# Performance work log

Hardware: AMD Instinct MI355X
Metric: run time of the kernel (lower is better)

## Reference

```python
import jax, jax.numpy as jnp
import numpy as np

NHEAD = 16
HEAD_DIM = 64
ROPE_BASE = 10000.0


def _rotate_half(x):
    # interleaved convention: pairs (x0,x1)->(-x1,x0)
    x1 = x[..., ::2]
    x2 = x[..., 1::2]
    return jnp.stack([-x2, x1], axis=-1).reshape(x.shape)


def _rope_cache(seq_len, head_dim, base):
    half = head_dim // 2
    inv_freq = 1.0 / base ** (jnp.arange(half, dtype=jnp.float32) / float(half))
    t = jnp.arange(seq_len, dtype=jnp.float32)
    freqs = jnp.einsum('i,j->ij', t, inv_freq)          # [T, half]
    emb = jnp.concatenate([freqs, freqs], axis=-1)      # [T, D] (half-half cat, matches torch source)
    return jnp.cos(emb), jnp.sin(emb)


def setup_inputs() -> dict:
    key = jax.random.key(0)
    k1, k2, k3 = jax.random.split(key, 3)
    b, t, c = 2, 2048, 1024
    x = jax.random.normal(k1, (b, t, c), dtype=jnp.float32)
    # torch nn.Linear weights: [out_features, in_features], scaled like kaiming-uniform-ish
    W_qkv = jax.random.normal(k2, (3 * c, c), dtype=jnp.float32) / np.sqrt(c)
    W_out = jax.random.normal(k3, (c, c), dtype=jnp.float32) / np.sqrt(c)
    return {"x": x, "W_qkv": W_qkv, "W_out": W_out}


def reference(x, W_qkv, W_out):
    b, t, c = x.shape
    nh, hd = NHEAD, HEAD_DIM
    qkv = x @ W_qkv.T                                   # [b, t, 3c]
    q, k, v = jnp.split(qkv, 3, axis=-1)

    def to_heads(a):
        return a.reshape(b, t, nh, hd).transpose(0, 2, 1, 3)  # [b, nh, t, hd]

    q, k, v = to_heads(q), to_heads(k), to_heads(v)
    cos, sin = _rope_cache(t, hd, ROPE_BASE)            # [t, hd]
    cos = cos.astype(q.dtype)[None, None]
    sin = sin.astype(q.dtype)[None, None]
    q = q * cos + _rotate_half(q) * sin
    k = k * cos + _rotate_half(k) * sin

    scale = 1.0 / np.sqrt(hd).astype(np.float32)
    scores = jnp.einsum('bhqd,bhkd->bhqk', q, k) * scale
    attn = jax.nn.softmax(scores, axis=-1)
    y = jnp.einsum('bhqk,bhkd->bhqd', attn, v)          # [b, nh, t, hd]
    y = y.transpose(0, 2, 1, 3).reshape(b, t, c)
    return y @ W_out.T
```

## Files before the change

### kernel.cpp

```cpp
#include <hip/hip_runtime.h>
#include <hip/hip_bf16.h>
#include <math.h>

typedef __hip_bfloat16 bf16;
typedef _Float16 f16;
typedef __attribute__((ext_vector_type(8))) short bf16x8;
typedef __attribute__((ext_vector_type(8))) _Float16 f16x8;
typedef __attribute__((ext_vector_type(4))) float f32x4;
typedef __attribute__((ext_vector_type(4))) unsigned u32x4;

#define MFMA_BF(a,b,c) __builtin_amdgcn_mfma_f32_16x16x32_bf16((a),(b),(c),0,0,0)
#define MFMA_F16(a,b,c) __builtin_amdgcn_mfma_f32_16x16x32_f16((a),(b),(c),0,0,0)

__device__ __forceinline__ void load_lds16(const void* g, void* l) {
  __builtin_amdgcn_global_load_lds(
      (__attribute__((address_space(1))) void*)(g),
      (__attribute__((address_space(3))) void*)(l), 16, 0, 0);
}

__device__ __forceinline__ unsigned pk_bf16(float a, float b) {
  unsigned ua = __builtin_bit_cast(unsigned, a);
  unsigned ub = __builtin_bit_cast(unsigned, b);
  ua += 0x7fffu + ((ua >> 16) & 1u);
  ub += 0x7fffu + ((ub >> 16) & 1u);
  return (ua >> 16) | (ub & 0xffff0000u);
}

__global__ void cvt_all(const float* __restrict__ x, const float* __restrict__ wq,
                        const float* __restrict__ wo, unsigned* __restrict__ xb,
                        unsigned* __restrict__ wqb, unsigned* __restrict__ wob) {
  int i = blockIdx.x * blockDim.x + threadIdx.x;
  const float* src;
  unsigned* dst;
  int off;
  if (i < 1048576) { src = x; dst = xb; off = i; }
  else if (i < 1048576 + 786432) { src = wq; dst = wqb; off = i - 1048576; }
  else { src = wo; dst = wob; off = i - (1048576 + 786432); }
  float4 v = reinterpret_cast<const float4*>(src)[off];
  uint2 u;
  u.x = pk_bf16(v.x, v.y);
  u.y = pk_bf16(v.z, v.w);
  reinterpret_cast<uint2*>(dst)[off] = u;
}

__global__ __launch_bounds__(256, 2)
void gemm_qkv(const bf16* __restrict__ A, const bf16* __restrict__ B,
              bf16* __restrict__ outq, bf16* __restrict__ outk,
              f16* __restrict__ outv) {
  __shared__ __align__(16) bf16 As[128 * 32];
  __shared__ __align__(16) bf16 Bs[128 * 32];
  const int K = 1024;
  const int tid = threadIdx.x;
  const int w = tid >> 6;
  const int lane = tid & 63;
  const int quad = lane >> 4;
  const int col = lane & 15;
  const int waveM = w >> 1;
  const int waveN = w & 1;
  const int bm = blockIdx.y * 128;
  const int bn = blockIdx.x * 128;

  f32x4 acc[4][4] = {};
  const int srow = lane >> 2;
  const int skoff = (lane & 3) * 8;

  for (int k0 = 0; k0 < K; k0 += 32) {
    __syncthreads();
#pragma unroll
    for (int p = 0; p < 2; ++p) {
      int r = p * 64 + w * 16 + srow;
      load_lds16(A + (size_t)(bm + r) * K + k0 + skoff, (char*)As + p * 4096 + w * 1024);
      load_lds16(B + (size_t)(bn + r) * K + k0 + skoff, (char*)Bs + p * 4096 + w * 1024);
    }
    __syncthreads();
    bf16x8 af[4], bfr[4];
#pragma unroll
    for (int i = 0; i < 4; ++i)
      af[i] = *reinterpret_cast<const bf16x8*>(As + (waveM * 64 + i * 16 + col) * 32 + quad * 8);
#pragma unroll
    for (int j = 0; j < 4; ++j)
      bfr[j] = *reinterpret_cast<const bf16x8*>(Bs + (waveN * 64 + j * 16 + col) * 32 + quad * 8);
#pragma unroll
    for (int i = 0; i < 4; ++i)
#pragma unroll
      for (int j = 0; j < 4; ++j)
        acc[i][j] = MFMA_BF(af[i], bfr[j], acc[i][j]);
  }

  if (bn < 2048) {
    const float NEGK = -0.4152410118f;
    const float C1 = 0.1803368799f;
    const float sgn = (col & 1) ? 1.0f : -1.0f;
#pragma unroll
    for (int j = 0; j < 4; ++j) {
      const int n0 = bn + waveN * 64 + j * 16;
      const int sel = n0 >> 10;
      const int hh = (n0 & 1023) >> 6;
      const int dd = (n0 & 63) + col;
      bf16* outp = sel ? outk : outq;
      const float post = sel ? 1.0f : C1;
      const float invf = __builtin_amdgcn_exp2f((float)((n0 & 31) + col) * NEGK);
#pragma unroll
      for (int i = 0; i < 4; ++i) {
#pragma unroll
        for (int r = 0; r < 4; ++r) {
          int m = bm + waveM * 64 + i * 16 + quad * 4 + r;
          int b = m >> 11, t = m & 2047;
          float v = acc[i][j][r];
          float partner = __shfl_xor(v, 1);
          float ang = (float)t * invf;
          float res = (v * __cosf(ang) + sgn * partner * __sinf(ang)) * post;
          outp[((size_t)(b * 16 + hh) * 2048 + t) * 64 + dd] = __float2bfloat16(res);
        }
      }
    }
  } else {
    const int b = bm >> 11;
    const int tt0 = (bm & 2047) + waveM * 64;
#pragma unroll
    for (int j = 0; j < 4; ++j) {
      const int n0 = bn + waveN * 64 + j * 16;
      const int hh = (n0 & 1023) >> 6;
      const int dd = (n0 & 63) + col;
      f16* dst = outv + (size_t)(b * 16 + hh) * 131072 + (size_t)dd * 2048;
#pragma unroll
      for (int i = 0; i < 4; ++i) {
        uint2 pk;
        pk.x = __builtin_bit_cast(unsigned, __builtin_amdgcn_cvt_pkrtz(acc[i][j][0], acc[i][j][1]));
        pk.y = __builtin_bit_cast(unsigned, __builtin_amdgcn_cvt_pkrtz(acc[i][j][2], acc[i][j][3]));
        *reinterpret_cast<uint2*>(dst + tt0 + i * 16 + quad * 4) = pk;
      }
    }
  }
}

__global__ __launch_bounds__(256, 2)
void gemm_out(const bf16* __restrict__ A, const bf16* __restrict__ B,
              float* __restrict__ outf) {
  __shared__ __align__(16) bf16 As[64 * 32];
  __shared__ __align__(16) bf16 Bs[128 * 32];
  const int K = 1024;
  const int tid = threadIdx.x;
  const int w = tid >> 6;
  const int lane = tid & 63;
  const int quad = lane >> 4;
  const int col = lane & 15;
  const int bm = blockIdx.y * 64;
  const int bn = blockIdx.x * 128;

  f32x4 acc[4][2] = {};
  const int srow = lane >> 2;
  const int skoff = (lane & 3) * 8;

  for (int k0 = 0; k0 < K; k0 += 32) {
    __syncthreads();
    load_lds16(A + (size_t)(bm + w * 16 + srow) * K + k0 + skoff, (char*)As + w * 1024);
#pragma unroll
    for (int p = 0; p < 2; ++p)
      load_lds16(B + (size_t)(bn + p * 64 + w * 16 + srow) * K + k0 + skoff,
                 (char*)Bs + p * 4096 + w * 1024);
    __syncthreads();
    bf16x8 af[4], bfr[2];
#pragma unroll
    for (int i = 0; i < 4; ++i)
      af[i] = *reinterpret_cast<const bf16x8*>(As + (i * 16 + col) * 32 + quad * 8);
#pragma unroll
    for (int j = 0; j < 2; ++j)
      bfr[j] = *reinterpret_cast<const bf16x8*>(Bs + (w * 32 + j * 16 + col) * 32 + quad * 8);
#pragma unroll
    for (int i = 0; i < 4; ++i)
#pragma unroll
      for (int j = 0; j < 2; ++j)
        acc[i][j] = MFMA_BF(af[i], bfr[j], acc[i][j]);
  }

#pragma unroll
  for (int i = 0; i < 4; ++i)
#pragma unroll
    for (int j = 0; j < 2; ++j) {
      const int n0 = bn + w * 32 + j * 16;
#pragma unroll
      for (int r = 0; r < 4; ++r) {
        int m = bm + i * 16 + quad * 4 + r;
        outf[(size_t)m * 1024 + n0 + col] = acc[i][j][r];
      }
    }
}

__global__ __launch_bounds__(256, 4)
void attn_kernel(const bf16* __restrict__ qh, const bf16* __restrict__ kh,
                 const f16* __restrict__ vt, bf16* __restrict__ O1,
                 bf16* __restrict__ O2, float* __restrict__ lw) {
  __shared__ __align__(16) bf16 Ks[2][64 * 64];
  __shared__ __align__(16) f16 Vs[2][64 * 64];

  const int bh = blockIdx.z;
  const int split = blockIdx.y;
  const int kc0 = split << 10;
  const int w = threadIdx.x >> 6;
  const int lane = threadIdx.x & 63;
  const int quad = lane >> 4;
  const int col = lane & 15;

  const int qrow0 = blockIdx.x * 128 + w * 32 + col;
  bf16x8 qf[2][2];
#pragma unroll
  for (int f = 0; f < 2; ++f)
#pragma unroll
    for (int c = 0; c < 2; ++c)
      qf[f][c] = *reinterpret_cast<const bf16x8*>(
          qh + ((size_t)bh * 2048 + qrow0 + f * 16) * 64 + c * 32 + quad * 8);

  const int s8 = lane >> 3;
  const int blk = (lane & 7) ^ s8;
  const bf16* kg = kh + (size_t)bh * 2048 * 64;
  const f16* vg = vt + (size_t)bh * 64 * 2048;
  char* klds0 = (char*)&Ks[0][0] + w * 2048;
  char* vlds0 = (char*)&Vs[0][0] + w * 2048;
  const int ks0 = 32 * (w >> 1) + 8 * ((4 * w + (s8 >> 2)) & 3) + 4 * (w & 1) + (s8 & 3);
  const int ks1 = 32 * (w >> 1) + 8 * ((4 * w + 2 + (s8 >> 2)) & 3) + 4 * (w & 1) + (s8 & 3);
  const int vrow0 = w * 16 + s8;

  const int csw = col & 7;
  const int sw0 = (quad ^ csw) * 8;
  const int sw1 = ((quad + 4) ^ csw) * 8;
  const int rdbase = col * 64;

  f32x4 O[2][4] = {};
  float l[2] = {};

  load_lds16(kg + (size_t)(kc0 + ks0) * 64 + blk * 8, klds0);
  load_lds16(kg + (size_t)(kc0 + ks1) * 64 + blk * 8, klds0 + 1024);
  load_lds16(vg + (size_t)vrow0 * 2048 + kc0 + blk * 8, vlds0);
  load_lds16(vg + (size_t)(vrow0 + 8) * 2048 + kc0 + blk * 8, vlds0 + 1024);

  int buf = 0;
  const int kend = kc0 + 1024;
  for (int kc = kc0; kc < kend; kc += 64) {
    __asm__ volatile("s_waitcnt vmcnt(0)" ::: "memory");
    __asm__ volatile("s_barrier" ::: "memory");
    if (kc + 64 < kend) {
      const int nb = buf ^ 1;
      const int kn = kc + 64;
      load_lds16(kg + (size_t)(kn + ks0) * 64 + blk * 8, klds0 + nb * 8192);
      load_lds16(kg + (size_t)(kn + ks1) * 64 + blk * 8, klds0 + nb * 8192 + 1024);
      load_lds16(vg + (size_t)vrow0 * 2048 + kn + blk * 8, vlds0 + nb * 8192);
      load_lds16(vg + (size_t)(vrow0 + 8) * 2048 + kn + blk * 8, vlds0 + nb * 8192 + 1024);
    }

    const bf16* kt = &Ks[buf][0];
    const f16* vtile = &Vs[buf][0];

    f32x4 s[2][4];
#pragma unroll
    for (int t = 0; t < 4; ++t) {
      bf16x8 kf0 = *reinterpret_cast<const bf16x8*>(kt + t * 1024 + rdbase + sw0);
      bf16x8 kf1 = *reinterpret_cast<const bf16x8*>(kt + t * 1024 + rdbase + sw1);
#pragma unroll
      for (int f = 0; f < 2; ++f) {
        f32x4 a = {};
        a = MFMA_BF(kf0, qf[f][0], a);
        a = MFMA_BF(kf1, qf[f][1], a);
        s[f][t] = a;
      }
    }

    f16x8 pf[2][2];
#pragma unroll
    for (int f = 0; f < 2; ++f) {
      unsigned pk[8];
      float lf = 0.0f;
#pragma unroll
      for (int t = 0; t < 4; ++t) {
        float p0 = __builtin_amdgcn_exp2f(s[f][t][0]);
        float p1 = __builtin_amdgcn_exp2f(s[f][t][1]);
        float p2 = __builtin_amdgcn_exp2f(s[f][t][2]);
        float p3 = __builtin_amdgcn_exp2f(s[f][t][3]);
        lf += (p0 + p1) + (p2 + p3);
        pk[t * 2]     = __builtin_bit_cast(unsigned, __builtin_amdgcn_cvt_pkrtz(p0, p1));
        pk[t * 2 + 1] = __builtin_bit_cast(unsigned, __builtin_amdgcn_cvt_pkrtz(p2, p3));
      }
      l[f] += lf;
      pf[f][0] = __builtin_bit_cast(f16x8, (u32x4){pk[0], pk[1], pk[2], pk[3]});
      pf[f][1] = __builtin_bit_cast(f16x8, (u32x4){pk[4], pk[5], pk[6], pk[7]});
    }

#pragma unroll
    for (int j = 0; j < 4; ++j) {
      f16x8 vf0 = *reinterpret_cast<const f16x8*>(vtile + j * 1024 + rdbase + sw0);
      f16x8 vf1 = *reinterpret_cast<const f16x8*>(vtile + j * 1024 + rdbase + sw1);
#pragma unroll
      for (int f = 0; f < 2; ++f) {
        O[f][j] = MFMA_F16(vf0, pf[f][0], O[f][j]);
        O[f][j] = MFMA_F16(vf1, pf[f][1], O[f][j]);
      }
    }
    buf ^= 1;
  }

  bf16* o_out = split ? O2 : O1;
  float* lrow = lw + split * 65536 + bh * 2048;
  const int b = bh >> 4, h = bh & 15;
#pragma unroll
  for (int f = 0; f < 2; ++f) {
    float lv = l[f];
    lv += __shfl_xor(lv, 16, 64);
    lv += __shfl_xor(lv, 32, 64);
    int tq = blockIdx.x * 128 + w * 32 + f * 16 + col;
    if (lane < 16) lrow[tq] = lv;
    size_t base = ((size_t)b * 2048 + tq) * 1024 + h * 64;
#pragma unroll
    for (int j = 0; j < 4; ++j) {
      uint2 pk2;
      pk2.x = pk_bf16(O[f][j][0], O[f][j][1]);
      pk2.y = pk_bf16(O[f][j][2], O[f][j][3]);
      *reinterpret_cast<uint2*>((unsigned short*)o_out + base + j * 16 + quad * 4) = pk2;
    }
  }
}

__global__ void merge_y(const bf16* __restrict__ O1, const bf16* __restrict__ O2,
                        const float* __restrict__ lw, bf16* __restrict__ y) {
  int i = blockIdx.x * blockDim.x + threadIdx.x;
  int c8 = i & 127;
  int t = (i >> 7) & 2047;
  int b = i >> 18;
  int bh = b * 16 + (c8 >> 3);
  float inv = 1.0f / (lw[bh * 2048 + t] + lw[65536 + bh * 2048 + t]);
  size_t off = (size_t)i * 8;
  ushort4 a1 = *reinterpret_cast<const ushort4*>((const unsigned short*)O1 + off);
  ushort4 a2 = *reinterpret_cast<const ushort4*>((const unsigned short*)O2 + off);
  ushort4 b1 = *reinterpret_cast<const ushort4*>((const unsigned short*)O1 + off + 4);
  ushort4 b2 = *reinterpret_cast<const ushort4*>((const unsigned short*)O2 + off + 4);
  const unsigned short* u1 = &a1.x;
  const unsigned short* u2 = &a2.x;
  const unsigned short* v1 = &b1.x;
  const unsigned short* v2 = &b2.x;
  float o[8];
#pragma unroll
  for (int e = 0; e < 4; ++e) {
    float s1 = __builtin_bit_cast(float, (unsigned)u1[e] << 16) +
               __builtin_bit_cast(float, (unsigned)u2[e] << 16);
    float s2 = __builtin_bit_cast(float, (unsigned)v1[e] << 16) +
               __builtin_bit_cast(float, (unsigned)v2[e] << 16);
    o[e] = s1 * inv;
    o[e + 4] = s2 * inv;
  }
  uint4 res;
  res.x = pk_bf16(o[0], o[1]);
  res.y = pk_bf16(o[2], o[3]);
  res.z = pk_bf16(o[4], o[5]);
  res.w = pk_bf16(o[6], o[7]);
  *reinterpret_cast<uint4*>((unsigned short*)y + off) = res;
}

extern "C" void kernel_launch(void* const* d_in, const int* in_sizes, int n_in,
                              void* d_out, int out_size, void* d_ws, size_t ws_size,
                              hipStream_t stream) {
  const float* x    = (const float*)d_in[0];
  const float* wqkv = (const float*)d_in[1];
  const float* wout = (const float*)d_in[2];
  float* out = (float*)d_out;
  char* ws = (char*)d_ws;

  bf16* xb    = (bf16*)(ws);
  bf16* wqkvb = (bf16*)(ws + (size_t)(8 << 20));
  bf16* woutb = (bf16*)(ws + (size_t)(14 << 20));
  bf16* qh    = (bf16*)(ws + (size_t)(16 << 20));
  bf16* kh    = (bf16*)(ws + (size_t)(24 << 20));
  f16*  vt    = (f16*) (ws + (size_t)(32 << 20));
  bf16* O1    = (bf16*)(ws + (size_t)(40 << 20));
  bf16* O2    = (bf16*)(ws);
  float* lw   = (float*)(ws + (size_t)(8 << 20));
  bf16* y     = (bf16*)(ws + (size_t)(16 << 20));

  cvt_all<<<8192, 256, 0, stream>>>(x, wqkv, wout,
                                    (unsigned*)xb, (unsigned*)wqkvb, (unsigned*)woutb);
  gemm_qkv<<<dim3(24, 32), 256, 0, stream>>>(xb, wqkvb, qh, kh, vt);
  attn_kernel<<<dim3(16, 2, 32), 256, 0, stream>>>(qh, kh, vt, O1, O2, lw);
  merge_y<<<2048, 256, 0, stream>>>(O1, O2, lw, y);
  gemm_out<<<dim3(8, 64), 256, 0, stream>>>(y, woutb, out);
}
```

Measured before the change: 198.4 us.

## Triple-buffer GEMM and attention loads, swizzle LDS, drop split-K merge kernel

```diff
diff --git a/kernel.cpp b/kernel.cpp
--- a/kernel.cpp
+++ b/kernel.cpp
@@ -47,8 +47,8 @@
 void gemm_qkv(const bf16* __restrict__ A, const bf16* __restrict__ B,
               bf16* __restrict__ outq, bf16* __restrict__ outk,
               f16* __restrict__ outv) {
-  __shared__ __align__(16) bf16 As[128 * 32];
-  __shared__ __align__(16) bf16 Bs[128 * 32];
+  __shared__ __align__(16) bf16 As[3][128 * 32];
+  __shared__ __align__(16) bf16 Bs[3][128 * 32];
   const int K = 1024;
   const int tid = threadIdx.x;
   const int w = tid >> 6;
@@ -62,29 +62,47 @@
 
   f32x4 acc[4][4] = {};
   const int srow = lane >> 2;
-  const int skoff = (lane & 3) * 8;
-
-  for (int k0 = 0; k0 < K; k0 += 32) {
-    __syncthreads();
+  const int skoff = (((lane & 3) ^ ((srow >> 1) & 3))) * 8;
+  const int swq = (quad ^ ((col >> 1) & 3)) * 8;
+
+  auto stage = [&](int k0, int sb) {
 #pragma unroll
     for (int p = 0; p < 2; ++p) {
       int r = p * 64 + w * 16 + srow;
-      load_lds16(A + (size_t)(bm + r) * K + k0 + skoff, (char*)As + p * 4096 + w * 1024);
-      load_lds16(B + (size_t)(bn + r) * K + k0 + skoff, (char*)Bs + p * 4096 + w * 1024);
-    }
-    __syncthreads();
+      load_lds16(A + (size_t)(bm + r) * K + k0 + skoff,
+                 (char*)As + sb * 8192 + p * 4096 + w * 1024);
+      load_lds16(B + (size_t)(bn + r) * K + k0 + skoff,
+                 (char*)Bs + sb * 8192 + p * 4096 + w * 1024);
+    }
+  };
+
+  stage(0, 0);
+  stage(32, 1);
+
+  int cb = 0;
+  for (int k0 = 0; k0 < K; k0 += 32) {
+    if (k0 + 32 < K) __asm__ volatile("s_waitcnt vmcnt(4)" ::: "memory");
+    else             __asm__ volatile("s_waitcnt vmcnt(0)" ::: "memory");
+    __asm__ volatile("s_barrier" ::: "memory");
+    if (k0 + 64 < K) {
+      int nb = cb + 2; if (nb >= 3) nb -= 3;
+      stage(k0 + 64, nb);
+    }
+    const bf16* at = &As[cb][0];
+    const bf16* bt = &Bs[cb][0];
     bf16x8 af[4], bfr[4];
 #pragma unroll
     for (int i = 0; i < 4; ++i)
-      af[i] = *reinterpret_cast<const bf16x8*>(As + (waveM * 64 + i * 16 + col) * 32 + quad * 8);
+      af[i] = *reinterpret_cast<const bf16x8*>(at + (waveM * 64 + i * 16 + col) * 32 + swq);
 #pragma unroll
     for (int j = 0; j < 4; ++j)
-      bfr[j] = *reinterpret_cast<const bf16x8*>(Bs + (waveN * 64 + j * 16 + col) * 32 + quad * 8);
+      bfr[j] = *reinterpret_cast<const bf16x8*>(bt + (waveN * 64 + j * 16 + col) * 32 + swq);
 #pragma unroll
     for (int i = 0; i < 4; ++i)
 #pragma unroll
       for (int j = 0; j < 4; ++j)
         acc[i][j] = MFMA_BF(af[i], bfr[j], acc[i][j]);
+    cb = (cb == 2) ? 0 : cb + 1;
   }
 
   if (bn < 2048) {
@@ -137,8 +155,8 @@
 __global__ __launch_bounds__(256, 2)
 void gemm_out(const bf16* __restrict__ A, const bf16* __restrict__ B,
               float* __restrict__ outf) {
-  __shared__ __align__(16) bf16 As[64 * 32];
-  __shared__ __align__(16) bf16 Bs[128 * 32];
+  __shared__ __align__(16) bf16 As[3][64 * 32];
+  __shared__ __align__(16) bf16 Bs[3][128 * 32];
   const int K = 1024;
   const int tid = threadIdx.x;
   const int w = tid >> 6;
@@ -150,28 +168,45 @@
 
   f32x4 acc[4][2] = {};
   const int srow = lane >> 2;
-  const int skoff = (lane & 3) * 8;
-
-  for (int k0 = 0; k0 < K; k0 += 32) {
-    __syncthreads();
-    load_lds16(A + (size_t)(bm + w * 16 + srow) * K + k0 + skoff, (char*)As + w * 1024);
+  const int skoff = (((lane & 3) ^ ((srow >> 1) & 3))) * 8;
+  const int swq = (quad ^ ((col >> 1) & 3)) * 8;
+
+  auto stage = [&](int k0, int sb) {
+    load_lds16(A + (size_t)(bm + w * 16 + srow) * K + k0 + skoff,
+               (char*)As + sb * 4096 + w * 1024);
 #pragma unroll
     for (int p = 0; p < 2; ++p)
       load_lds16(B + (size_t)(bn + p * 64 + w * 16 + srow) * K + k0 + skoff,
-                 (char*)Bs + p * 4096 + w * 1024);
-    __syncthreads();
+                 (char*)Bs + sb * 8192 + p * 4096 + w * 1024);
+  };
+
+  stage(0, 0);
+  stage(32, 1);
+
+  int cb = 0;
+  for (int k0 = 0; k0 < K; k0 += 32) {
+    if (k0 + 32 < K) __asm__ volatile("s_waitcnt vmcnt(3)" ::: "memory");
+    else             __asm__ volatile("s_waitcnt vmcnt(0)" ::: "memory");
+    __asm__ volatile("s_barrier" ::: "memory");
+    if (k0 + 64 < K) {
+      int nb = cb + 2; if (nb >= 3) nb -= 3;
+      stage(k0 + 64, nb);
+    }
+    const bf16* at = &As[cb][0];
+    const bf16* bt = &Bs[cb][0];
     bf16x8 af[4], bfr[2];
 #pragma unroll
     for (int i = 0; i < 4; ++i)
-      af[i] = *reinterpret_cast<const bf16x8*>(As + (i * 16 + col) * 32 + quad * 8);
+      af[i] = *reinterpret_cast<const bf16x8*>(at + (i * 16 + col) * 32 + swq);
 #pragma unroll
     for (int j = 0; j < 2; ++j)
-      bfr[j] = *reinterpret_cast<const bf16x8*>(Bs + (w * 32 + j * 16 + col) * 32 + quad * 8);
+      bfr[j] = *reinterpret_cast<const bf16x8*>(bt + (w * 32 + j * 16 + col) * 32 + swq);
 #pragma unroll
     for (int i = 0; i < 4; ++i)
 #pragma unroll
       for (int j = 0; j < 2; ++j)
         acc[i][j] = MFMA_BF(af[i], bfr[j], acc[i][j]);
+    cb = (cb == 2) ? 0 : cb + 1;
   }
 
 #pragma unroll
@@ -187,16 +222,13 @@
     }
 }
 
-__global__ __launch_bounds__(256, 4)
+__global__ __launch_bounds__(256, 3)
 void attn_kernel(const bf16* __restrict__ qh, const bf16* __restrict__ kh,
-                 const f16* __restrict__ vt, bf16* __restrict__ O1,
-                 bf16* __restrict__ O2, float* __restrict__ lw) {
-  __shared__ __align__(16) bf16 Ks[2][64 * 64];
-  __shared__ __align__(16) f16 Vs[2][64 * 64];
-
-  const int bh = blockIdx.z;
-  const int split = blockIdx.y;
-  const int kc0 = split << 10;
+                 const f16* __restrict__ vt, bf16* __restrict__ y) {
+  __shared__ __align__(16) bf16 Ks[3][64 * 64];
+  __shared__ __align__(16) f16 Vs[3][64 * 64];
+
+  const int bh = blockIdx.y;
   const int w = threadIdx.x >> 6;
   const int lane = threadIdx.x & 63;
   const int quad = lane >> 4;
@@ -215,8 +247,6 @@
   const int blk = (lane & 7) ^ s8;
   const bf16* kg = kh + (size_t)bh * 2048 * 64;
   const f16* vg = vt + (size_t)bh * 64 * 2048;
-  char* klds0 = (char*)&Ks[0][0] + w * 2048;
-  char* vlds0 = (char*)&Vs[0][0] + w * 2048;
   const int ks0 = 32 * (w >> 1) + 8 * ((4 * w + (s8 >> 2)) & 3) + 4 * (w & 1) + (s8 & 3);
   const int ks1 = 32 * (w >> 1) + 8 * ((4 * w + 2 + (s8 >> 2)) & 3) + 4 * (w & 1) + (s8 & 3);
   const int vrow0 = w * 16 + s8;
@@ -229,27 +259,30 @@
   f32x4 O[2][4] = {};
   float l[2] = {};
 
-  load_lds16(kg + (size_t)(kc0 + ks0) * 64 + blk * 8, klds0);
-  load_lds16(kg + (size_t)(kc0 + ks1) * 64 + blk * 8, klds0 + 1024);
-  load_lds16(vg + (size_t)vrow0 * 2048 + kc0 + blk * 8, vlds0);
-  load_lds16(vg + (size_t)(vrow0 + 8) * 2048 + kc0 + blk * 8, vlds0 + 1024);
-
-  int buf = 0;
-  const int kend = kc0 + 1024;
-  for (int kc = kc0; kc < kend; kc += 64) {
-    __asm__ volatile("s_waitcnt vmcnt(0)" ::: "memory");
+  auto stage = [&](int kn, int sb) {
+    char* kb = (char*)Ks + sb * 8192 + w * 2048;
+    char* vb = (char*)Vs + sb * 8192 + w * 2048;
+    load_lds16(kg + (size_t)(kn + ks0) * 64 + blk * 8, kb);
+    load_lds16(kg + (size_t)(kn + ks1) * 64 + blk * 8, kb + 1024);
+    load_lds16(vg + (size_t)vrow0 * 2048 + kn + blk * 8, vb);
+    load_lds16(vg + (size_t)(vrow0 + 8) * 2048 + kn + blk * 8, vb + 1024);
+  };
+
+  stage(0, 0);
+  stage(64, 1);
+
+  int cb = 0;
+  for (int kc = 0; kc < 2048; kc += 64) {
+    if (kc + 64 < 2048) __asm__ volatile("s_waitcnt vmcnt(4)" ::: "memory");
+    else                __asm__ volatile("s_waitcnt vmcnt(0)" ::: "memory");
     __asm__ volatile("s_barrier" ::: "memory");
-    if (kc + 64 < kend) {
-      const int nb = buf ^ 1;
-      const int kn = kc + 64;
-      load_lds16(kg + (size_t)(kn + ks0) * 64 + blk * 8, klds0 + nb * 8192);
-      load_lds16(kg + (size_t)(kn + ks1) * 64 + blk * 8, klds0 + nb * 8192 + 1024);
-      load_lds16(vg + (size_t)vrow0 * 2048 + kn + blk * 8, vlds0 + nb * 8192);
-      load_lds16(vg + (size_t)(vrow0 + 8) * 2048 + kn + blk * 8, vlds0 + nb * 8192 + 1024);
-    }
-
-    const bf16* kt = &Ks[buf][0];
-    const f16* vtile = &Vs[buf][0];
+    if (kc + 128 < 2048) {
+      int nb = cb + 2; if (nb >= 3) nb -= 3;
+      stage(kc + 128, nb);
+    }
+
+    const bf16* kt = &Ks[cb][0];
+    const f16* vtile = &Vs[cb][0];
 
     f32x4 s[2][4];
 #pragma unroll
@@ -295,63 +328,26 @@
         O[f][j] = MFMA_F16(vf1, pf[f][1], O[f][j]);
       }
     }
-    buf ^= 1;
-  }
-
-  bf16* o_out = split ? O2 : O1;
-  float* lrow = lw + split * 65536 + bh * 2048;
+    cb = (cb == 2) ? 0 : cb + 1;
+  }
+
   const int b = bh >> 4, h = bh & 15;
 #pragma unroll
   for (int f = 0; f < 2; ++f) {
     float lv = l[f];
     lv += __shfl_xor(lv, 16, 64);
     lv += __shfl_xor(lv, 32, 64);
+    float inv = 1.0f / lv;
     int tq = blockIdx.x * 128 + w * 32 + f * 16 + col;
-    if (lane < 16) lrow[tq] = lv;
     size_t base = ((size_t)b * 2048 + tq) * 1024 + h * 64;
 #pragma unroll
     for (int j = 0; j < 4; ++j) {
       uint2 pk2;
-      pk2.x = pk_bf16(O[f][j][0], O[f][j][1]);
-      pk2.y = pk_bf16(O[f][j][2], O[f][j][3]);
-      *reinterpret_cast<uint2*>((unsigned short*)o_out + base + j * 16 + quad * 4) = pk2;
-    }
-  }
-}
-
-__global__ void merge_y(const bf16* __restrict__ O1, const bf16* __restrict__ O2,
-                        const float* __restrict__ lw, bf16* __restrict__ y) {
-  int i = blockIdx.x * blockDim.x + threadIdx.x;
-  int c8 = i & 127;
-  int t = (i >> 7) & 2047;
-  int b = i >> 18;
-  int bh = b * 16 + (c8 >> 3);
-  float inv = 1.0f / (lw[bh * 2048 + t] + lw[65536 + bh * 2048 + t]);
-  size_t off = (size_t)i * 8;
-  ushort4 a1 = *reinterpret_cast<const ushort4*>((const unsigned short*)O1 + off);
-  ushort4 a2 = *reinterpret_cast<const ushort4*>((const unsigned short*)O2 + off);
-  ushort4 b1 = *reinterpret_cast<const ushort4*>((const unsigned short*)O1 + off + 4);
-  ushort4 b2 = *reinterpret_cast<const ushort4*>((const unsigned short*)O2 + off + 4);
-  const unsigned short* u1 = &a1.x;
-  const unsigned short* u2 = &a2.x;
-  const unsigned short* v1 = &b1.x;
-  const unsigned short* v2 = &b2.x;
-  float o[8];
-#pragma unroll
-  for (int e = 0; e < 4; ++e) {
-    float s1 = __builtin_bit_cast(float, (unsigned)u1[e] << 16) +
-               __builtin_bit_cast(float, (unsigned)u2[e] << 16);
-    float s2 = __builtin_bit_cast(float, (unsigned)v1[e] << 16) +
-               __builtin_bit_cast(float, (unsigned)v2[e] << 16);
-    o[e] = s1 * inv;
-    o[e + 4] = s2 * inv;
-  }
-  uint4 res;
-  res.x = pk_bf16(o[0], o[1]);
-  res.y = pk_bf16(o[2], o[3]);
-  res.z = pk_bf16(o[4], o[5]);
-  res.w = pk_bf16(o[6], o[7]);
-  *reinterpret_cast<uint4*>((unsigned short*)y + off) = res;
+      pk2.x = pk_bf16(O[f][j][0] * inv, O[f][j][1] * inv);
+      pk2.y = pk_bf16(O[f][j][2] * inv, O[f][j][3] * inv);
+      *reinterpret_cast<uint2*>((unsigned short*)y + base + j * 16 + quad * 4) = pk2;
+    }
+  }
 }
 
 extern "C" void kernel_launch(void* const* d_in, const int* in_sizes, int n_in,
@@ -369,15 +365,11 @@
   bf16* qh    = (bf16*)(ws + (size_t)(16 << 20));
   bf16* kh    = (bf16*)(ws + (size_t)(24 << 20));
   f16*  vt    = (f16*) (ws + (size_t)(32 << 20));
-  bf16* O1    = (bf16*)(ws + (size_t)(40 << 20));
-  bf16* O2    = (bf16*)(ws);
-  float* lw   = (float*)(ws + (size_t)(8 << 20));
-  bf16* y     = (bf16*)(ws + (size_t)(16 << 20));
+  bf16* y     = (bf16*)(ws + (size_t)(40 << 20));
 
   cvt_all<<<8192, 256, 0, stream>>>(x, wqkv, wout,
                                     (unsigned*)xb, (unsigned*)wqkvb, (unsigned*)woutb);
   gemm_qkv<<<dim3(24, 32), 256, 0, stream>>>(xb, wqkvb, qh, kh, vt);
-  attn_kernel<<<dim3(16, 2, 32), 256, 0, stream>>>(qh, kh, vt, O1, O2, lw);
-  merge_y<<<2048, 256, 0, stream>>>(O1, O2, lw, y);
+  attn_kernel<<<dim3(16, 32), 256, 0, stream>>>(qh, kh, vt, y);
   gemm_out<<<dim3(8, 64), 256, 0, stream>>>(y, woutb, out);
 }
```

Result: faster. 178.0 us (-10.3%).
